# Kernel optimization log

Measured on AMD Instinct MI355X. Metric: run time of the kernel, lower is better.

The kernel has to match this reference:

```python
import jax, jax.numpy as jnp
import numpy as np

EPS = 1e-8  # matches TMLoss(eps=1e-08)


def setup_inputs() -> dict:
    key = jax.random.key(0)
    k1, k2 = jax.random.split(key)
    b, n = 2048, 1024
    # pseudo protein coords: spread out like real structures (~tens of Angstroms)
    pred = jax.random.normal(k1, (b, n, 3), dtype=jnp.float32) * 10.0
    # native coords = pred + noise, arbitrarily rotated/translated is fine since we Kabsch-align
    actual = pred + jax.random.normal(k2, (b, n, 3), dtype=jnp.float32)
    return {"predicted_coords": pred, "actual_coords": actual}


def _kabsch_align(align_to, align_from):
    """Rigidly align align_from onto align_to (batched Kabsch). Shapes (b,n,3)."""
    mu_to = jnp.mean(align_to, axis=1, keepdims=True)
    mu_from = jnp.mean(align_from, axis=1, keepdims=True)
    p = align_to - mu_to      # (b,n,3) target, centered
    q = align_from - mu_from  # (b,n,3) mobile, centered
    # 3x3 cross-covariance M = q^T p; optimal R maximizes tr(R^T M)
    M = jnp.einsum('bni,bnj->bij', q, p)  # (b,3,3)
    U, S, Vt = jnp.linalg.svd(M)
    # proper-rotation (det=+1) correction on smallest singular direction
    d = jnp.sign(jnp.linalg.det(U) * jnp.linalg.det(Vt))  # (b,)
    ones = jnp.ones_like(d)
    D = jnp.stack([ones, ones, d], axis=-1)               # (b,3)
    R = jnp.einsum('bik,bk,bkj->bij', U, D, Vt)           # (b,3,3)
    aligned = jnp.einsum('bni,bij->bnj', q, R) + mu_to    # (b,n,3)
    return align_to, aligned


def _calc_tm(dev, reduce=True):
    """dev: (b,n) per-residue deviations -> TM-score."""
    n = dev.shape[-1]
    d0 = 1.24 * (n - 15.0) ** (1.0 / 3.0) - 1.8
    tm = jnp.mean(1.0 / (1.0 + (dev / d0) ** 2), axis=-1)  # (b,)
    return jnp.mean(tm) if reduce else tm


def reference(predicted_coords, actual_coords):
    # align=True path: Kabsch-align native onto prediction
    _, aligned_actual = _kabsch_align(predicted_coords, actual_coords)
    # per-residue deviation (eps added elementwise before norm, as in torch source)
    dev = jnp.linalg.norm(predicted_coords - aligned_actual + EPS, axis=-1)  # (b,n)
    return -_calc_tm(dev, reduce=True)
```

## Files before the change

### kernel.cpp

```cpp
#include <hip/hip_runtime.h>
#include <math.h>

#define NRES 1024
#define TM_EPS 1e-8f

__global__ void tm_reduce1(const float* __restrict__ pred, const float* __restrict__ act,
                           float* __restrict__ sums) {
    int b = blockIdx.x;
    const float4* p4 = (const float4*)(pred + (size_t)b * NRES * 3);
    const float4* a4 = (const float4*)(act  + (size_t)b * NRES * 3);
    int t = threadIdx.x;

    float4 pf0 = p4[3 * t + 0], pf1 = p4[3 * t + 1], pf2 = p4[3 * t + 2];
    float4 af0 = a4[3 * t + 0], af1 = a4[3 * t + 1], af2 = a4[3 * t + 2];

    float px[4] = {pf0.x, pf0.w, pf1.z, pf2.y};
    float py[4] = {pf0.y, pf1.x, pf1.w, pf2.z};
    float pz[4] = {pf0.z, pf1.y, pf2.x, pf2.w};
    float ax[4] = {af0.x, af0.w, af1.z, af2.y};
    float ay[4] = {af0.y, af1.x, af1.w, af2.z};
    float az[4] = {af0.z, af1.y, af2.x, af2.w};

    float acc[15];
#pragma unroll
    for (int i = 0; i < 15; i++) acc[i] = 0.f;
#pragma unroll
    for (int r = 0; r < 4; r++) {
        acc[0] += px[r]; acc[1] += py[r]; acc[2] += pz[r];
        acc[3] += ax[r]; acc[4] += ay[r]; acc[5] += az[r];
        acc[6]  += ax[r] * px[r]; acc[7]  += ax[r] * py[r]; acc[8]  += ax[r] * pz[r];
        acc[9]  += ay[r] * px[r]; acc[10] += ay[r] * py[r]; acc[11] += ay[r] * pz[r];
        acc[12] += az[r] * px[r]; acc[13] += az[r] * py[r]; acc[14] += az[r] * pz[r];
    }

#pragma unroll
    for (int off = 32; off > 0; off >>= 1) {
#pragma unroll
        for (int i = 0; i < 15; i++) acc[i] += __shfl_down(acc[i], off);
    }
    __shared__ float red[4][15];
    int wave = threadIdx.x >> 6, lane = threadIdx.x & 63;
    if (lane == 0) {
#pragma unroll
        for (int i = 0; i < 15; i++) red[wave][i] = acc[i];
    }
    __syncthreads();
    if (threadIdx.x < 15) {
        int i = threadIdx.x;
        sums[(size_t)b * 16 + i] = red[0][i] + red[1][i] + red[2][i] + red[3][i];
    }
}

__global__ void tm_kabsch(const float* __restrict__ sums, float* __restrict__ rot, int B) {
    int b = blockIdx.x * blockDim.x + threadIdx.x;
    if (b >= B) return;
    const float* s = sums + (size_t)b * 16;
    const double n = (double)NRES;
    double mp[3], mq[3];
#pragma unroll
    for (int i = 0; i < 3; i++) { mp[i] = (double)s[i] / n; mq[i] = (double)s[3 + i] / n; }
    double M[3][3];
#pragma unroll
    for (int i = 0; i < 3; i++)
#pragma unroll
        for (int j = 0; j < 3; j++)
            M[i][j] = (double)s[6 + i * 3 + j] - n * mq[i] * mp[j];

    double Sxx = M[0][0], Sxy = M[0][1], Sxz = M[0][2];
    double Syx = M[1][0], Syy = M[1][1], Syz = M[1][2];
    double Szx = M[2][0], Szy = M[2][1], Szz = M[2][2];
    double K[4][4];
    K[0][0] = Sxx + Syy + Szz; K[0][1] = Syz - Szy;        K[0][2] = Szx - Sxz;         K[0][3] = Sxy - Syx;
    K[1][0] = K[0][1];         K[1][1] = Sxx - Syy - Szz;  K[1][2] = Sxy + Syx;         K[1][3] = Szx + Sxz;
    K[2][0] = K[0][2];         K[2][1] = K[1][2];          K[2][2] = -Sxx + Syy - Szz;  K[2][3] = Syz + Szy;
    K[3][0] = K[0][3];         K[3][1] = K[1][3];          K[3][2] = K[2][3];           K[3][3] = -Sxx - Syy + Szz;

    double K2[4][4];
#pragma unroll
    for (int i = 0; i < 4; i++)
#pragma unroll
        for (int j = 0; j < 4; j++) {
            double acc = 0.0;
#pragma unroll
            for (int k = 0; k < 4; k++) acc += K[i][k] * K[k][j];
            K2[i][j] = acc;
        }
    double p2 = 0.0, p3 = 0.0, p4 = 0.0;
#pragma unroll
    for (int i = 0; i < 4; i++)
#pragma unroll
        for (int j = 0; j < 4; j++) {
            p2 += K[i][j] * K[i][j];
            p3 += K2[i][j] * K[i][j];
            p4 += K2[i][j] * K2[i][j];
        }
    double e2 = -0.5 * p2;
    double e3 = p3 / 3.0;
    double e4 = (0.5 * p2 * p2 - p4) * 0.25;

    double lam = sqrt(p2);
#pragma unroll
    for (int it = 0; it < 20; it++) {
        double lam2 = lam * lam;
        double P  = lam2 * lam2 + e2 * lam2 - e3 * lam + e4;
        double Pp = 4.0 * lam * lam2 + 2.0 * e2 * lam - e3;
        lam -= P / Pp;
    }

    double Bm[4][4];
#pragma unroll
    for (int i = 0; i < 4; i++)
#pragma unroll
        for (int j = 0; j < 4; j++) Bm[i][j] = K[i][j] - ((i == j) ? lam : 0.0);

    double cand[4][4];
#pragma unroll
    for (int r = 0; r < 4; r++) {
        int rr[3];
        int k = 0;
#pragma unroll
        for (int i = 0; i < 4; i++) if (i != r) rr[k++] = i;
#pragma unroll
        for (int c = 0; c < 4; c++) {
            int cc[3];
            int m = 0;
#pragma unroll
            for (int j = 0; j < 4; j++) if (j != c) cc[m++] = j;
            double d =
                Bm[rr[0]][cc[0]] * (Bm[rr[1]][cc[1]] * Bm[rr[2]][cc[2]] - Bm[rr[1]][cc[2]] * Bm[rr[2]][cc[1]])
              - Bm[rr[0]][cc[1]] * (Bm[rr[1]][cc[0]] * Bm[rr[2]][cc[2]] - Bm[rr[1]][cc[2]] * Bm[rr[2]][cc[0]])
              + Bm[rr[0]][cc[2]] * (Bm[rr[1]][cc[0]] * Bm[rr[2]][cc[1]] - Bm[rr[1]][cc[1]] * Bm[rr[2]][cc[0]]);
            cand[r][c] = (((r + c) & 1) ? -d : d);
        }
    }
    int bestr = 0;
    double bestn = -1.0;
#pragma unroll
    for (int r = 0; r < 4; r++) {
        double nn = cand[r][0] * cand[r][0] + cand[r][1] * cand[r][1] +
                    cand[r][2] * cand[r][2] + cand[r][3] * cand[r][3];
        if (nn > bestn) { bestn = nn; bestr = r; }
    }
    double w = cand[bestr][0], x = cand[bestr][1], y = cand[bestr][2], z = cand[bestr][3];
    double nrm = sqrt(w * w + x * x + y * y + z * z);
    w /= nrm; x /= nrm; y /= nrm; z /= nrm;

    double A[3][3];
    A[0][0] = 1.0 - 2.0 * (y * y + z * z); A[0][1] = 2.0 * (x * y - w * z);       A[0][2] = 2.0 * (x * z + w * y);
    A[1][0] = 2.0 * (x * y + w * z);       A[1][1] = 1.0 - 2.0 * (x * x + z * z); A[1][2] = 2.0 * (y * z - w * x);
    A[2][0] = 2.0 * (x * z - w * y);       A[2][1] = 2.0 * (y * z + w * x);       A[2][2] = 1.0 - 2.0 * (x * x + y * y);

    float* o = rot + (size_t)b * 12;
#pragma unroll
    for (int i = 0; i < 3; i++)
#pragma unroll
        for (int j = 0; j < 3; j++) o[i * 3 + j] = (float)A[i][j];
#pragma unroll
    for (int i = 0; i < 3; i++)
        o[9 + i] = (float)(mp[i] - (A[i][0] * mq[0] + A[i][1] * mq[1] + A[i][2] * mq[2]));
}

__global__ void tm_score(const float* __restrict__ pred, const float* __restrict__ act,
                         const float* __restrict__ rot, float* __restrict__ out,
                         float scale, float inv_d02) {
    int b = blockIdx.x;
    const float* R = rot + (size_t)b * 12;
    float A00 = R[0], A01 = R[1], A02 = R[2];
    float A10 = R[3], A11 = R[4], A12 = R[5];
    float A20 = R[6], A21 = R[7], A22 = R[8];
    float t0 = R[9], t1 = R[10], t2 = R[11];

    const float4* p4 = (const float4*)(pred + (size_t)b * NRES * 3);
    const float4* a4 = (const float4*)(act  + (size_t)b * NRES * 3);
    int t = threadIdx.x;
    float4 pf0 = p4[3 * t + 0], pf1 = p4[3 * t + 1], pf2 = p4[3 * t + 2];
    float4 af0 = a4[3 * t + 0], af1 = a4[3 * t + 1], af2 = a4[3 * t + 2];

    float px[4] = {pf0.x, pf0.w, pf1.z, pf2.y};
    float py[4] = {pf0.y, pf1.x, pf1.w, pf2.z};
    float pz[4] = {pf0.z, pf1.y, pf2.x, pf2.w};
    float ax[4] = {af0.x, af0.w, af1.z, af2.y};
    float ay[4] = {af0.y, af1.x, af1.w, af2.z};
    float az[4] = {af0.z, af1.y, af2.x, af2.w};

    float s = 0.f;
#pragma unroll
    for (int r = 0; r < 4; r++) {
        float dx = px[r] - (A00 * ax[r] + A01 * ay[r] + A02 * az[r]) - t0 + TM_EPS;
        float dy = py[r] - (A10 * ax[r] + A11 * ay[r] + A12 * az[r]) - t1 + TM_EPS;
        float dz = pz[r] - (A20 * ax[r] + A21 * ay[r] + A22 * az[r]) - t2 + TM_EPS;
        float d2 = dx * dx + dy * dy + dz * dz;
        s += 1.0f / (1.0f + d2 * inv_d02);
    }
#pragma unroll
    for (int off = 32; off > 0; off >>= 1) s += __shfl_down(s, off);

    __shared__ float red[4];
    int wave = threadIdx.x >> 6, lane = threadIdx.x & 63;
    if (lane == 0) red[wave] = s;
    __syncthreads();
    if (threadIdx.x == 0) {
        float tot = red[0] + red[1] + red[2] + red[3];
        atomicAdd(out, -tot * scale);
    }
}

extern "C" void kernel_launch(void* const* d_in, const int* in_sizes, int n_in,
                              void* d_out, int out_size, void* d_ws, size_t ws_size,
                              hipStream_t stream) {
    const float* pred = (const float*)d_in[0];
    const float* act  = (const float*)d_in[1];
    float* out = (float*)d_out;
    int B = in_sizes[0] / (NRES * 3);

    float* ws   = (float*)d_ws;
    float* sums = ws;
    float* rot  = ws + (size_t)B * 16;

    hipMemsetAsync(d_out, 0, sizeof(float), stream);

    tm_reduce1<<<B, 256, 0, stream>>>(pred, act, sums);
    tm_kabsch<<<(B + 255) / 256, 256, 0, stream>>>(sums, rot, B);

    double d0 = 1.24 * cbrt((double)NRES - 15.0) - 1.8;
    float inv_d02 = (float)(1.0 / (d0 * d0));
    float scale = 1.0f / ((float)B * (float)NRES);
    tm_score<<<B, 256, 0, stream>>>(pred, act, rot, out, scale, inv_d02);
}
```

Measured before the change: 120.3 us.

## Fuse reduction, Kabsch solve, and scoring into one kernel with shared-memory staging

Merges the three kernels into a single per-batch block. Coordinates are loaded once and staged in shared memory for the scoring pass, and thread 0 runs the double-precision quaternion eigen-solve, broadcasting the rotation through shared memory. This removes the second global read of both inputs and two kernel launches. In exchange, all other threads sit idle during the serial fp64 solve on one lane, and the Newton iteration count is cut from 20 to 14.

```diff
diff --git a/kernel.cpp b/kernel.cpp
--- a/kernel.cpp
+++ b/kernel.cpp
@@ -4,203 +4,197 @@
 #define NRES 1024
 #define TM_EPS 1e-8f
 
-__global__ void tm_reduce1(const float* __restrict__ pred, const float* __restrict__ act,
-                           float* __restrict__ sums) {
+__global__ __launch_bounds__(256, 2) void tm_fused(const float* __restrict__ pred,
+                                                   const float* __restrict__ act,
+                                                   float* __restrict__ out,
+                                                   float scale, float inv_d02) {
+    __shared__ float4 sh[6][256];
+    __shared__ float red[4][15];
+    __shared__ float rotsh[12];
+
     int b = blockIdx.x;
+    int t = threadIdx.x;
     const float4* p4 = (const float4*)(pred + (size_t)b * NRES * 3);
     const float4* a4 = (const float4*)(act  + (size_t)b * NRES * 3);
-    int t = threadIdx.x;
 
     float4 pf0 = p4[3 * t + 0], pf1 = p4[3 * t + 1], pf2 = p4[3 * t + 2];
     float4 af0 = a4[3 * t + 0], af1 = a4[3 * t + 1], af2 = a4[3 * t + 2];
-
-    float px[4] = {pf0.x, pf0.w, pf1.z, pf2.y};
-    float py[4] = {pf0.y, pf1.x, pf1.w, pf2.z};
-    float pz[4] = {pf0.z, pf1.y, pf2.x, pf2.w};
-    float ax[4] = {af0.x, af0.w, af1.z, af2.y};
-    float ay[4] = {af0.y, af1.x, af1.w, af2.z};
-    float az[4] = {af0.z, af1.y, af2.x, af2.w};
-
-    float acc[15];
-#pragma unroll
-    for (int i = 0; i < 15; i++) acc[i] = 0.f;
-#pragma unroll
-    for (int r = 0; r < 4; r++) {
-        acc[0] += px[r]; acc[1] += py[r]; acc[2] += pz[r];
-        acc[3] += ax[r]; acc[4] += ay[r]; acc[5] += az[r];
-        acc[6]  += ax[r] * px[r]; acc[7]  += ax[r] * py[r]; acc[8]  += ax[r] * pz[r];
-        acc[9]  += ay[r] * px[r]; acc[10] += ay[r] * py[r]; acc[11] += ay[r] * pz[r];
-        acc[12] += az[r] * px[r]; acc[13] += az[r] * py[r]; acc[14] += az[r] * pz[r];
-    }
-
-#pragma unroll
-    for (int off = 32; off > 0; off >>= 1) {
-#pragma unroll
-        for (int i = 0; i < 15; i++) acc[i] += __shfl_down(acc[i], off);
-    }
-    __shared__ float red[4][15];
-    int wave = threadIdx.x >> 6, lane = threadIdx.x & 63;
-    if (lane == 0) {
-#pragma unroll
-        for (int i = 0; i < 15; i++) red[wave][i] = acc[i];
+    sh[0][t] = pf0; sh[1][t] = pf1; sh[2][t] = pf2;
+    sh[3][t] = af0; sh[4][t] = af1; sh[5][t] = af2;
+
+    {
+        float px[4] = {pf0.x, pf0.w, pf1.z, pf2.y};
+        float py[4] = {pf0.y, pf1.x, pf1.w, pf2.z};
+        float pz[4] = {pf0.z, pf1.y, pf2.x, pf2.w};
+        float ax[4] = {af0.x, af0.w, af1.z, af2.y};
+        float ay[4] = {af0.y, af1.x, af1.w, af2.z};
+        float az[4] = {af0.z, af1.y, af2.x, af2.w};
+
+        float acc[15];
+#pragma unroll
+        for (int i = 0; i < 15; i++) acc[i] = 0.f;
+#pragma unroll
+        for (int r = 0; r < 4; r++) {
+            acc[0] += px[r]; acc[1] += py[r]; acc[2] += pz[r];
+            acc[3] += ax[r]; acc[4] += ay[r]; acc[5] += az[r];
+            acc[6]  += ax[r] * px[r]; acc[7]  += ax[r] * py[r]; acc[8]  += ax[r] * pz[r];
+            acc[9]  += ay[r] * px[r]; acc[10] += ay[r] * py[r]; acc[11] += ay[r] * pz[r];
+            acc[12] += az[r] * px[r]; acc[13] += az[r] * py[r]; acc[14] += az[r] * pz[r];
+        }
+#pragma unroll
+        for (int off = 32; off > 0; off >>= 1) {
+#pragma unroll
+            for (int i = 0; i < 15; i++) acc[i] += __shfl_down(acc[i], off);
+        }
+        int wave = t >> 6, lane = t & 63;
+        if (lane == 0) {
+#pragma unroll
+            for (int i = 0; i < 15; i++) red[wave][i] = acc[i];
+        }
     }
     __syncthreads();
-    if (threadIdx.x < 15) {
-        int i = threadIdx.x;
-        sums[(size_t)b * 16 + i] = red[0][i] + red[1][i] + red[2][i] + red[3][i];
-    }
-}
-
-__global__ void tm_kabsch(const float* __restrict__ sums, float* __restrict__ rot, int B) {
-    int b = blockIdx.x * blockDim.x + threadIdx.x;
-    if (b >= B) return;
-    const float* s = sums + (size_t)b * 16;
-    const double n = (double)NRES;
-    double mp[3], mq[3];
-#pragma unroll
-    for (int i = 0; i < 3; i++) { mp[i] = (double)s[i] / n; mq[i] = (double)s[3 + i] / n; }
-    double M[3][3];
-#pragma unroll
-    for (int i = 0; i < 3; i++)
-#pragma unroll
-        for (int j = 0; j < 3; j++)
-            M[i][j] = (double)s[6 + i * 3 + j] - n * mq[i] * mp[j];
-
-    double Sxx = M[0][0], Sxy = M[0][1], Sxz = M[0][2];
-    double Syx = M[1][0], Syy = M[1][1], Syz = M[1][2];
-    double Szx = M[2][0], Szy = M[2][1], Szz = M[2][2];
-    double K[4][4];
-    K[0][0] = Sxx + Syy + Szz; K[0][1] = Syz - Szy;        K[0][2] = Szx - Sxz;         K[0][3] = Sxy - Syx;
-    K[1][0] = K[0][1];         K[1][1] = Sxx - Syy - Szz;  K[1][2] = Sxy + Syx;         K[1][3] = Szx + Sxz;
-    K[2][0] = K[0][2];         K[2][1] = K[1][2];          K[2][2] = -Sxx + Syy - Szz;  K[2][3] = Syz + Szy;
-    K[3][0] = K[0][3];         K[3][1] = K[1][3];          K[3][2] = K[2][3];           K[3][3] = -Sxx - Syy + Szz;
-
-    double K2[4][4];
-#pragma unroll
-    for (int i = 0; i < 4; i++)
-#pragma unroll
-        for (int j = 0; j < 4; j++) {
-            double acc = 0.0;
-#pragma unroll
-            for (int k = 0; k < 4; k++) acc += K[i][k] * K[k][j];
-            K2[i][j] = acc;
-        }
-    double p2 = 0.0, p3 = 0.0, p4 = 0.0;
-#pragma unroll
-    for (int i = 0; i < 4; i++)
-#pragma unroll
-        for (int j = 0; j < 4; j++) {
-            p2 += K[i][j] * K[i][j];
-            p3 += K2[i][j] * K[i][j];
-            p4 += K2[i][j] * K2[i][j];
-        }
-    double e2 = -0.5 * p2;
-    double e3 = p3 / 3.0;
-    double e4 = (0.5 * p2 * p2 - p4) * 0.25;
-
-    double lam = sqrt(p2);
-#pragma unroll
-    for (int it = 0; it < 20; it++) {
-        double lam2 = lam * lam;
-        double P  = lam2 * lam2 + e2 * lam2 - e3 * lam + e4;
-        double Pp = 4.0 * lam * lam2 + 2.0 * e2 * lam - e3;
-        lam -= P / Pp;
-    }
-
-    double Bm[4][4];
-#pragma unroll
-    for (int i = 0; i < 4; i++)
-#pragma unroll
-        for (int j = 0; j < 4; j++) Bm[i][j] = K[i][j] - ((i == j) ? lam : 0.0);
-
-    double cand[4][4];
-#pragma unroll
-    for (int r = 0; r < 4; r++) {
-        int rr[3];
-        int k = 0;
-#pragma unroll
-        for (int i = 0; i < 4; i++) if (i != r) rr[k++] = i;
-#pragma unroll
-        for (int c = 0; c < 4; c++) {
-            int cc[3];
-            int m = 0;
-#pragma unroll
-            for (int j = 0; j < 4; j++) if (j != c) cc[m++] = j;
-            double d =
-                Bm[rr[0]][cc[0]] * (Bm[rr[1]][cc[1]] * Bm[rr[2]][cc[2]] - Bm[rr[1]][cc[2]] * Bm[rr[2]][cc[1]])
-              - Bm[rr[0]][cc[1]] * (Bm[rr[1]][cc[0]] * Bm[rr[2]][cc[2]] - Bm[rr[1]][cc[2]] * Bm[rr[2]][cc[0]])
-              + Bm[rr[0]][cc[2]] * (Bm[rr[1]][cc[0]] * Bm[rr[2]][cc[1]] - Bm[rr[1]][cc[1]] * Bm[rr[2]][cc[0]]);
-            cand[r][c] = (((r + c) & 1) ? -d : d);
-        }
-    }
-    int bestr = 0;
-    double bestn = -1.0;
-#pragma unroll
-    for (int r = 0; r < 4; r++) {
-        double nn = cand[r][0] * cand[r][0] + cand[r][1] * cand[r][1] +
-                    cand[r][2] * cand[r][2] + cand[r][3] * cand[r][3];
-        if (nn > bestn) { bestn = nn; bestr = r; }
-    }
-    double w = cand[bestr][0], x = cand[bestr][1], y = cand[bestr][2], z = cand[bestr][3];
-    double nrm = sqrt(w * w + x * x + y * y + z * z);
-    w /= nrm; x /= nrm; y /= nrm; z /= nrm;
-
-    double A[3][3];
-    A[0][0] = 1.0 - 2.0 * (y * y + z * z); A[0][1] = 2.0 * (x * y - w * z);       A[0][2] = 2.0 * (x * z + w * y);
-    A[1][0] = 2.0 * (x * y + w * z);       A[1][1] = 1.0 - 2.0 * (x * x + z * z); A[1][2] = 2.0 * (y * z - w * x);
-    A[2][0] = 2.0 * (x * z - w * y);       A[2][1] = 2.0 * (y * z + w * x);       A[2][2] = 1.0 - 2.0 * (x * x + y * y);
-
-    float* o = rot + (size_t)b * 12;
-#pragma unroll
-    for (int i = 0; i < 3; i++)
-#pragma unroll
-        for (int j = 0; j < 3; j++) o[i * 3 + j] = (float)A[i][j];
-#pragma unroll
-    for (int i = 0; i < 3; i++)
-        o[9 + i] = (float)(mp[i] - (A[i][0] * mq[0] + A[i][1] * mq[1] + A[i][2] * mq[2]));
-}
-
-__global__ void tm_score(const float* __restrict__ pred, const float* __restrict__ act,
-                         const float* __restrict__ rot, float* __restrict__ out,
-                         float scale, float inv_d02) {
-    int b = blockIdx.x;
-    const float* R = rot + (size_t)b * 12;
-    float A00 = R[0], A01 = R[1], A02 = R[2];
-    float A10 = R[3], A11 = R[4], A12 = R[5];
-    float A20 = R[6], A21 = R[7], A22 = R[8];
-    float t0 = R[9], t1 = R[10], t2 = R[11];
-
-    const float4* p4 = (const float4*)(pred + (size_t)b * NRES * 3);
-    const float4* a4 = (const float4*)(act  + (size_t)b * NRES * 3);
-    int t = threadIdx.x;
-    float4 pf0 = p4[3 * t + 0], pf1 = p4[3 * t + 1], pf2 = p4[3 * t + 2];
-    float4 af0 = a4[3 * t + 0], af1 = a4[3 * t + 1], af2 = a4[3 * t + 2];
-
-    float px[4] = {pf0.x, pf0.w, pf1.z, pf2.y};
-    float py[4] = {pf0.y, pf1.x, pf1.w, pf2.z};
-    float pz[4] = {pf0.z, pf1.y, pf2.x, pf2.w};
-    float ax[4] = {af0.x, af0.w, af1.z, af2.y};
-    float ay[4] = {af0.y, af1.x, af1.w, af2.z};
-    float az[4] = {af0.z, af1.y, af2.x, af2.w};
-
-    float s = 0.f;
+
+    if (t == 0) {
+        float s[15];
+#pragma unroll
+        for (int i = 0; i < 15; i++) s[i] = red[0][i] + red[1][i] + red[2][i] + red[3][i];
+
+        const double n = (double)NRES;
+        double mp[3], mq[3];
+#pragma unroll
+        for (int i = 0; i < 3; i++) { mp[i] = (double)s[i] / n; mq[i] = (double)s[3 + i] / n; }
+        double M[3][3];
+#pragma unroll
+        for (int i = 0; i < 3; i++)
+#pragma unroll
+            for (int j = 0; j < 3; j++)
+                M[i][j] = (double)s[6 + i * 3 + j] - n * mq[i] * mp[j];
+
+        double Sxx = M[0][0], Sxy = M[0][1], Sxz = M[0][2];
+        double Syx = M[1][0], Syy = M[1][1], Syz = M[1][2];
+        double Szx = M[2][0], Szy = M[2][1], Szz = M[2][2];
+        double K[4][4];
+        K[0][0] = Sxx + Syy + Szz; K[0][1] = Syz - Szy;        K[0][2] = Szx - Sxz;         K[0][3] = Sxy - Syx;
+        K[1][0] = K[0][1];         K[1][1] = Sxx - Syy - Szz;  K[1][2] = Sxy + Syx;         K[1][3] = Szx + Sxz;
+        K[2][0] = K[0][2];         K[2][1] = K[1][2];          K[2][2] = -Sxx + Syy - Szz;  K[2][3] = Syz + Szy;
+        K[3][0] = K[0][3];         K[3][1] = K[1][3];          K[3][2] = K[2][3];           K[3][3] = -Sxx - Syy + Szz;
+
+        double K2[4][4];
+#pragma unroll
+        for (int i = 0; i < 4; i++)
+#pragma unroll
+            for (int j = 0; j < 4; j++) {
+                double acc = 0.0;
+#pragma unroll
+                for (int k = 0; k < 4; k++) acc += K[i][k] * K[k][j];
+                K2[i][j] = acc;
+            }
+        double p2 = 0.0, p3 = 0.0, p4s = 0.0;
+#pragma unroll
+        for (int i = 0; i < 4; i++)
+#pragma unroll
+            for (int j = 0; j < 4; j++) {
+                p2 += K[i][j] * K[i][j];
+                p3 += K2[i][j] * K[i][j];
+                p4s += K2[i][j] * K2[i][j];
+            }
+        double e2 = -0.5 * p2;
+        double e3 = p3 / 3.0;
+        double e4 = (0.5 * p2 * p2 - p4s) * 0.25;
+
+        double lam = sqrt(p2);
+#pragma unroll
+        for (int it = 0; it < 14; it++) {
+            double lam2 = lam * lam;
+            double P  = lam2 * lam2 + e2 * lam2 - e3 * lam + e4;
+            double Pp = 4.0 * lam * lam2 + 2.0 * e2 * lam - e3;
+            lam -= P / Pp;
+        }
+
+        double Bm[4][4];
+#pragma unroll
+        for (int i = 0; i < 4; i++)
+#pragma unroll
+            for (int j = 0; j < 4; j++) Bm[i][j] = K[i][j] - ((i == j) ? lam : 0.0);
+
+        double cand[4][4];
+#pragma unroll
+        for (int r = 0; r < 4; r++) {
+            int rr[3]; int k = 0;
+#pragma unroll
+            for (int i = 0; i < 4; i++) if (i != r) rr[k++] = i;
+#pragma unroll
+            for (int c = 0; c < 4; c++) {
+                int cc[3]; int m = 0;
+#pragma unroll
+                for (int j = 0; j < 4; j++) if (j != c) cc[m++] = j;
+                double d =
+                    Bm[rr[0]][cc[0]] * (Bm[rr[1]][cc[1]] * Bm[rr[2]][cc[2]] - Bm[rr[1]][cc[2]] * Bm[rr[2]][cc[1]])
+                  - Bm[rr[0]][cc[1]] * (Bm[rr[1]][cc[0]] * Bm[rr[2]][cc[2]] - Bm[rr[1]][cc[2]] * Bm[rr[2]][cc[0]])
+                  + Bm[rr[0]][cc[2]] * (Bm[rr[1]][cc[0]] * Bm[rr[2]][cc[1]] - Bm[rr[1]][cc[1]] * Bm[rr[2]][cc[0]]);
+                cand[r][c] = (((r + c) & 1) ? -d : d);
+            }
+        }
+        int bestr = 0;
+        double bestn = -1.0;
+#pragma unroll
+        for (int r = 0; r < 4; r++) {
+            double nn = cand[r][0] * cand[r][0] + cand[r][1] * cand[r][1] +
+                        cand[r][2] * cand[r][2] + cand[r][3] * cand[r][3];
+            if (nn > bestn) { bestn = nn; bestr = r; }
+        }
+        double w = cand[bestr][0], x = cand[bestr][1], y = cand[bestr][2], z = cand[bestr][3];
+        double nrm = sqrt(w * w + x * x + y * y + z * z);
+        w /= nrm; x /= nrm; y /= nrm; z /= nrm;
+
+        double A[3][3];
+        A[0][0] = 1.0 - 2.0 * (y * y + z * z); A[0][1] = 2.0 * (x * y - w * z);       A[0][2] = 2.0 * (x * z + w * y);
+        A[1][0] = 2.0 * (x * y + w * z);       A[1][1] = 1.0 - 2.0 * (x * x + z * z); A[1][2] = 2.0 * (y * z - w * x);
+        A[2][0] = 2.0 * (x * z - w * y);       A[2][1] = 2.0 * (y * z + w * x);       A[2][2] = 1.0 - 2.0 * (x * x + y * y);
+
+#pragma unroll
+        for (int i = 0; i < 3; i++)
+#pragma unroll
+            for (int j = 0; j < 3; j++) rotsh[i * 3 + j] = (float)A[i][j];
+#pragma unroll
+        for (int i = 0; i < 3; i++)
+            rotsh[9 + i] = (float)(mp[i] - (A[i][0] * mq[0] + A[i][1] * mq[1] + A[i][2] * mq[2]));
+    }
+    __syncthreads();
+
+    float A00 = rotsh[0], A01 = rotsh[1], A02 = rotsh[2];
+    float A10 = rotsh[3], A11 = rotsh[4], A12 = rotsh[5];
+    float A20 = rotsh[6], A21 = rotsh[7], A22 = rotsh[8];
+    float t0 = rotsh[9], t1 = rotsh[10], t2 = rotsh[11];
+
+    float4 qf0 = sh[0][t], qf1 = sh[1][t], qf2 = sh[2][t];
+    float4 bf0 = sh[3][t], bf1 = sh[4][t], bf2 = sh[5][t];
+
+    float px[4] = {qf0.x, qf0.w, qf1.z, qf2.y};
+    float py[4] = {qf0.y, qf1.x, qf1.w, qf2.z};
+    float pz[4] = {qf0.z, qf1.y, qf2.x, qf2.w};
+    float ax[4] = {bf0.x, bf0.w, bf1.z, bf2.y};
+    float ay[4] = {bf0.y, bf1.x, bf1.w, bf2.z};
+    float az[4] = {bf0.z, bf1.y, bf2.x, bf2.w};
+
+    float sc = 0.f;
 #pragma unroll
     for (int r = 0; r < 4; r++) {
         float dx = px[r] - (A00 * ax[r] + A01 * ay[r] + A02 * az[r]) - t0 + TM_EPS;
         float dy = py[r] - (A10 * ax[r] + A11 * ay[r] + A12 * az[r]) - t1 + TM_EPS;
         float dz = pz[r] - (A20 * ax[r] + A21 * ay[r] + A22 * az[r]) - t2 + TM_EPS;
         float d2 = dx * dx + dy * dy + dz * dz;
-        s += 1.0f / (1.0f + d2 * inv_d02);
-    }
-#pragma unroll
-    for (int off = 32; off > 0; off >>= 1) s += __shfl_down(s, off);
-
-    __shared__ float red[4];
-    int wave = threadIdx.x >> 6, lane = threadIdx.x & 63;
-    if (lane == 0) red[wave] = s;
+        sc += 1.0f / (1.0f + d2 * inv_d02);
+    }
+#pragma unroll
+    for (int off = 32; off > 0; off >>= 1) sc += __shfl_down(sc, off);
+
+    __shared__ float red2[4];
+    int wave = t >> 6, lane = t & 63;
+    if (lane == 0) red2[wave] = sc;
     __syncthreads();
-    if (threadIdx.x == 0) {
-        float tot = red[0] + red[1] + red[2] + red[3];
+    if (t == 0) {
+        float tot = red2[0] + red2[1] + red2[2] + red2[3];
         atomicAdd(out, -tot * scale);
     }
 }
@@ -213,17 +207,10 @@
     float* out = (float*)d_out;
     int B = in_sizes[0] / (NRES * 3);
 
-    float* ws   = (float*)d_ws;
-    float* sums = ws;
-    float* rot  = ws + (size_t)B * 16;
-
     hipMemsetAsync(d_out, 0, sizeof(float), stream);
-
-    tm_reduce1<<<B, 256, 0, stream>>>(pred, act, sums);
-    tm_kabsch<<<(B + 255) / 256, 256, 0, stream>>>(sums, rot, B);
 
     double d0 = 1.24 * cbrt((double)NRES - 15.0) - 1.8;
     float inv_d02 = (float)(1.0 / (d0 * d0));
     float scale = 1.0f / ((float)B * (float)NRES);
-    tm_score<<<B, 256, 0, stream>>>(pred, act, rot, out, scale, inv_d02);
+    tm_fused<<<B, 256, 0, stream>>>(pred, act, out, scale, inv_d02);
 }
```

New measurement: 110.1 us. 8.5% less time.
